# Optimization experiments

Measured on AMD Instinct MI355X. Metric: run time of the kernel, lower is better.

Reference implementation:

```python
import jax, jax.numpy as jnp
import numpy as np
from jax import lax

B = 8192
DEPTH = 4096
SCALES = 3
FLT = 4  # db2 filter length

_DB2_DEC_LO = np.array([-0.12940952255092145, 0.22414386804185735, 0.836516303737469, 0.48296291314469025], dtype=np.float32)
_DB2_DEC_HI = np.array([-0.48296291314469025, 0.836516303737469, 0.22414386804185735, 0.12940952255092145], dtype=np.float32)


def _coeff_lens(depth, flen, scales):
    # mirrors pywt.dwt_coeff_len(n, flen, 'zero') = floor((n + flen - 1) / 2)
    lens = [depth]
    for _ in range(scales):
        lens.append((lens[-1] + flen - 1) // 2)
    lens = lens[1:]
    lens.append(lens[-1])
    return lens  # e.g. [2049, 1026, 514, 514]

WAVE_DEPTH = int(np.sum(_coeff_lens(DEPTH, FLT, SCALES)))  # 4103


def setup_inputs() -> dict:
    key = jax.random.key(0)
    ks = jax.random.split(key, 5)
    x = jax.random.normal(ks[0], (B, DEPTH), dtype=jnp.float32)
    diag_b = 1.0 + 0.1 * jax.random.normal(ks[1], (DEPTH,), dtype=jnp.float32)
    diag_g = 1.0 + 0.1 * jax.random.normal(ks[2], (WAVE_DEPTH,), dtype=jnp.float32)
    diag_s = 1.0 + 0.1 * jax.random.normal(ks[3], (DEPTH,), dtype=jnp.float32)
    dec_lo = jnp.asarray(_DB2_DEC_LO)
    dec_hi = jnp.asarray(_DB2_DEC_HI)
    rec_lo = dec_lo[::-1]
    rec_hi = dec_hi[::-1]
    perm_idx = jax.random.permutation(ks[4], WAVE_DEPTH).astype(jnp.int32)
    return {"x": x, "diag_b": diag_b, "diag_g": diag_g, "diag_s": diag_s,
            "dec_lo": dec_lo, "dec_hi": dec_hi, "rec_lo": rec_lo, "rec_hi": rec_hi,
            "perm_idx": perm_idx}


def _forward(x, diag_b, diag_g, diag_s, dec_lo, dec_hi, rec_lo, rec_hi, perm_idx):
    L = dec_lo.shape[0]
    lens = _coeff_lens(x.shape[-1], L, SCALES)
    # mul_b: diag(vec) matmul == elementwise column scale
    a = x * diag_b
    # multi-level analysis DWT with 'zero' padding: full convolution, keep odd indices
    w_dec = jnp.stack([dec_lo[::-1], dec_hi[::-1]])[:, None, :]  # [2,1,L] (flip: lax does corr)
    details = []
    for _ in range(SCALES):
        y = lax.conv_general_dilated(a[:, None, :], w_dec, (2,), [(L - 2, L - 1)],
                                     dimension_numbers=("NCH", "OIH", "NCH"))
        a, d = y[:, 0, :], y[:, 1, :]
        details.append(d)
    c = jnp.concatenate([a] + details[::-1], axis=-1)  # [B, WAVE_DEPTH], [cA_s, cD_s, ..., cD_1]
    # mul_p: permutation matmul == column gather
    c = c[:, perm_idx]
    # mul_g
    c = c * diag_g
    # coefficient slicing exactly as in the original forward (incl. its start-update rule)
    rev = lens[::-1]
    coeffs = []
    start = 0
    for s_i in range(SCALES + 1):
        stop = start + rev[s_i]
        coeffs.append(c[:, start:stop])
        start = lens[s_i]
    # multi-level reconstruction (idwt, zero mode): zero-upsample, full conv, trim L-2 per side
    a = coeffs[0]
    w_rec = jnp.stack([rec_lo[::-1], rec_hi[::-1]])[None, :, :]  # [1,2,L]
    for d in coeffs[1:]:
        if a.shape[-1] == d.shape[-1] + 1:  # pywt waverec odd-length trim
            a = a[:, :-1]
        xin = jnp.stack([a, d], axis=1)  # [B,2,la]
        a = lax.conv_general_dilated(xin, w_rec, (1,), [(1, 1)], lhs_dilation=(2,),
                                     dimension_numbers=("NCH", "OIH", "NCH"))[:, 0, :]
    # mul_s
    return a * diag_s


def reference(x, diag_b, diag_g, diag_s, dec_lo, dec_hi, rec_lo, rec_hi, perm_idx):
    return _forward(x, diag_b, diag_g, diag_s, dec_lo, dec_hi, rec_lo, rec_hi, perm_idx)
```

## Files before the change

kernel.cpp:

```cpp
#include <hip/hip_runtime.h>


#define NT 512

__global__ __launch_bounds__(NT, 8) void wavelet_fused(
    const float* __restrict__ x,
    const float* __restrict__ diag_b,
    const float* __restrict__ diag_g,
    const float* __restrict__ diag_s,
    const float* __restrict__ dec_lo,
    const float* __restrict__ dec_hi,
    const float* __restrict__ rec_lo,
    const float* __restrict__ rec_hi,
    const int*   __restrict__ perm_idx,
    float* __restrict__ out)
{
    __shared__ __align__(16) float rawA[3088];
    __shared__ __align__(16) float rawC[4112];
    float* const A1 = rawA + 4;
    float* const A2 = rawA + 2060;
    float* const P  = rawA;
    float* const Cc = rawC;
    float* const R1 = rawC;

    const int tid = threadIdx.x;
    const long row = blockIdx.x;

    int4   pq0 = ((const int4*)perm_idx)[tid];
    float4 gq0 = ((const float4*)diag_g)[tid];
    int4   pq1; float4 gq1;
    if (tid < 128) {
        pq1 = ((const int4*)perm_idx)[512 + tid];
        gq1 = ((const float4*)diag_g)[512 + tid];
    }
    int pt = 0; float gt = 0.0f;
    if (tid < 3) { pt = perm_idx[2560 + tid]; gt = diag_g[2560 + tid]; }
    float4 sv0 = ((const float4*)diag_s)[2*tid];
    float4 sv1 = ((const float4*)diag_s)[2*tid + 1];

    const float lo0=dec_lo[0], lo1=dec_lo[1], lo2=dec_lo[2], lo3=dec_lo[3];
    const float hi0=dec_hi[0], hi1=dec_hi[1], hi2=dec_hi[2], hi3=dec_hi[3];
    const float rl0=rec_lo[0], rl1=rec_lo[1], rl2=rec_lo[2], rl3=rec_lo[3];
    const float rh0=rec_hi[0], rh1=rec_hi[1], rh2=rec_hi[2], rh3=rec_hi[3];

    if (tid < 2) rawA[2 + tid]    = 0.0f;
    if (tid < 3) rawA[2053 + tid] = 0.0f;
    if (tid < 2) rawA[2058 + tid] = 0.0f;
    if (tid < 2) rawA[3086 + tid] = 0.0f;

    {
        const float* xr = x + row * 4096;
        float4 xv0 = *(const float4*)(xr + 8*tid);
        float4 xv1 = *(const float4*)(xr + 8*tid + 4);
        float4 bv0 = *(const float4*)(diag_b + 8*tid);
        float4 bv1 = *(const float4*)(diag_b + 8*tid + 4);
        float vm2 = 0.0f, vm1 = 0.0f;
        if (tid > 0) {
            float2 xm = *(const float2*)(xr + 8*tid - 2);
            float2 bm = *(const float2*)(diag_b + 8*tid - 2);
            vm2 = xm.x * bm.x; vm1 = xm.y * bm.y;
        }
        float v0 = xv0.x*bv0.x, v1 = xv0.y*bv0.y, v2 = xv0.z*bv0.z, v3 = xv0.w*bv0.w;
        float v4 = xv1.x*bv1.x, v5 = xv1.y*bv1.y, v6 = xv1.z*bv1.z, v7 = xv1.w*bv1.w;
        float4 av, dv;
        av.x = lo0*v1 + lo1*v0 + lo2*vm1 + lo3*vm2;
        dv.x = hi0*v1 + hi1*v0 + hi2*vm1 + hi3*vm2;
        av.y = lo0*v3 + lo1*v2 + lo2*v1 + lo3*v0;
        dv.y = hi0*v3 + hi1*v2 + hi2*v1 + hi3*v0;
        av.z = lo0*v5 + lo1*v4 + lo2*v3 + lo3*v2;
        dv.z = hi0*v5 + hi1*v4 + hi2*v3 + hi3*v2;
        av.w = lo0*v7 + lo1*v6 + lo2*v5 + lo3*v4;
        dv.w = hi0*v7 + hi1*v6 + hi2*v5 + hi3*v4;
        *(float4*)(A1 + 4*tid) = av;
        *(float4*)(Cc + 2056 + 4*tid) = dv;
        if (tid == 0) {
            float xa = xr[4094]*diag_b[4094], xb = xr[4095]*diag_b[4095];
            A1[2048]        = lo2*xb + lo3*xa;
            Cc[2056 + 2048] = hi2*xb + hi3*xa;
        }
    }
    __syncthreads();

    for (int p = tid; p < 513; p += NT) {
        float2 u0 = *(const float2*)(A1 + 4*p - 2);
        float4 u1 = *(const float4*)(A1 + 4*p);
        float2 ap, dp;
        ap.x = lo0*u1.y + lo1*u1.x + lo2*u0.y + lo3*u0.x;
        dp.x = hi0*u1.y + hi1*u1.x + hi2*u0.y + hi3*u0.x;
        ap.y = lo0*u1.w + lo1*u1.z + lo2*u1.y + lo3*u1.x;
        dp.y = hi0*u1.w + hi1*u1.z + hi2*u1.y + hi3*u1.x;
        *(float2*)(A2 + 2*p)        = ap;
        *(float2*)(Cc + 1028 + 2*p) = dp;
    }
    __syncthreads();

    for (int p = tid; p < 257; p += NT) {
        float2 u0 = *(const float2*)(A2 + 4*p - 2);
        float4 u1 = *(const float4*)(A2 + 4*p);
        float2 ap, dp;
        ap.x = lo0*u1.y + lo1*u1.x + lo2*u0.y + lo3*u0.x;
        dp.x = hi0*u1.y + hi1*u1.x + hi2*u0.y + hi3*u0.x;
        ap.y = lo0*u1.w + lo1*u1.z + lo2*u1.y + lo3*u1.x;
        dp.y = hi0*u1.w + hi1*u1.z + hi2*u1.y + hi3*u1.x;
        *(float2*)(Cc + 2*p)       = ap;
        *(float2*)(Cc + 514 + 2*p) = dp;
    }
    __syncthreads();

    {
        float4 cv;
        cv.x = Cc[pq0.x + (pq0.x >= 2054 ? 2 : 0)] * gq0.x;
        cv.y = Cc[pq0.y + (pq0.y >= 2054 ? 2 : 0)] * gq0.y;
        cv.z = Cc[pq0.z + (pq0.z >= 2054 ? 2 : 0)] * gq0.z;
        cv.w = Cc[pq0.w + (pq0.w >= 2054 ? 2 : 0)] * gq0.w;
        *(float4*)(P + 4*tid) = cv;
        if (tid < 128) {
            float4 cw;
            cw.x = Cc[pq1.x + (pq1.x >= 2054 ? 2 : 0)] * gq1.x;
            cw.y = Cc[pq1.y + (pq1.y >= 2054 ? 2 : 0)] * gq1.y;
            cw.z = Cc[pq1.z + (pq1.z >= 2054 ? 2 : 0)] * gq1.z;
            cw.w = Cc[pq1.w + (pq1.w >= 2054 ? 2 : 0)] * gq1.w;
            *(float4*)(P + 2048 + 4*tid) = cw;
        }
        if (tid < 3)  P[2560 + tid] = Cc[pt + (pt >= 2054 ? 2 : 0)] * gt;
        if (tid == 3) P[2563] = 0.0f;
    }
    __syncthreads();

    if (tid < 257) {
        int p0 = 2 * tid;
        float a0v = P[p0],        a1v = P[p0 + 1],    a2v = P[p0 + 2];
        float d0v = P[2049 + p0], d1v = P[2050 + p0], d2v = P[2051 + p0];
        float4 w;
        w.x = rl2*a0v + rl0*a1v + rh2*d0v + rh0*d1v;
        w.y = rl3*a0v + rl1*a1v + rh3*d0v + rh1*d1v;
        w.z = rl2*a1v + rl0*a2v + rh2*d1v + rh0*d2v;
        w.w = rl3*a1v + rl1*a2v + rh3*d1v + rh1*d2v;
        if (tid < 256) *(float4*)(R1 + 4*tid) = w;
        else           { R1[1024] = w.x; R1[1025] = w.y; }
    }
    __syncthreads();

    {
        const int u = tid;
        float2 q01 = *(const float2*)(R1 + 2*u);
        float2 q23 = *(const float2*)(R1 + 2*u + 2);
        float2 ea  = *(const float2*)(P + 1026 + 2*u);
        float2 eb  = *(const float2*)(P + 1028 + 2*u);
        float e0 = ea.x, e1 = ea.y, e2 = eb.x, e3 = eb.y;
        float s0  = rl2*q01.x + rl0*q01.y + rh2*e0 + rh0*e1;
        float s1v = rl3*q01.x + rl1*q01.y + rh3*e0 + rh1*e1;
        float s2v = rl2*q01.y + rl0*q23.x + rh2*e1 + rh0*e2;
        float s3v = rl3*q01.y + rl1*q23.x + rh3*e1 + rh1*e2;
        float s4  = rl2*q23.x + rl0*q23.y + rh2*e2 + rh0*e3;
        float2 fa = *(const float2*)(P + 514 + 4*u);
        float2 fb = *(const float2*)(P + 516 + 4*u);
        float  f4 = P[518 + 4*u];
        float f0 = fa.x, f1 = fa.y, f2 = fb.x, f3 = fb.y;
        float4 o0, o1;
        o0.x = (rl2*s0  + rl0*s1v + rh2*f0 + rh0*f1) * sv0.x;
        o0.y = (rl3*s0  + rl1*s1v + rh3*f0 + rh1*f1) * sv0.y;
        o0.z = (rl2*s1v + rl0*s2v + rh2*f1 + rh0*f2) * sv0.z;
        o0.w = (rl3*s1v + rl1*s2v + rh3*f1 + rh1*f2) * sv0.w;
        o1.x = (rl2*s2v + rl0*s3v + rh2*f2 + rh0*f3) * sv1.x;
        o1.y = (rl3*s2v + rl1*s3v + rh3*f2 + rh1*f3) * sv1.y;
        o1.z = (rl2*s3v + rl0*s4  + rh2*f3 + rh0*f4) * sv1.z;
        o1.w = (rl3*s3v + rl1*s4  + rh3*f3 + rh1*f4) * sv1.w;
        float4* outr = (float4*)(out + row * 4096);
        outr[2*u]     = o0;
        outr[2*u + 1] = o1;
    }
}

extern "C" void kernel_launch(void* const* d_in, const int* in_sizes, int n_in,
                              void* d_out, int out_size, void* d_ws, size_t ws_size,
                              hipStream_t stream) {
    const float* x       = (const float*)d_in[0];
    const float* diag_b  = (const float*)d_in[1];
    const float* diag_g  = (const float*)d_in[2];
    const float* diag_s  = (const float*)d_in[3];
    const float* dec_lo  = (const float*)d_in[4];
    const float* dec_hi  = (const float*)d_in[5];
    const float* rec_lo  = (const float*)d_in[6];
    const float* rec_hi  = (const float*)d_in[7];
    const int*   perm    = (const int*)d_in[8];
    float* out = (float*)d_out;

    const int B = in_sizes[0] / 4096;
    wavelet_fused<<<B, NT, 0, stream>>>(
        x, diag_b, diag_g, diag_s, dec_lo, dec_hi, rec_lo, rec_hi, perm, out);
}
```

Measured before the change: 261.3 us.

## Compose DWT levels 2-3 into one 10-tap pass and fuse reconstruction levels

Levels two and three of the analysis are merged into a single pass using precomputed composite 10-tap low/high filters applied to the level-1 approximation. Level-2 details are still computed per thread. On the synthesis side, the first reconstruction level is computed in registers inside the second, which removes its shared-memory round trip. This drops two barriers and the A2 buffer, shrinking shared memory, at the cost of redundant FMAs and a few extra boundary special cases.

```diff
diff --git a/kernel.cpp b/kernel.cpp
--- a/kernel.cpp
+++ b/kernel.cpp
@@ -15,13 +15,11 @@
     const int*   __restrict__ perm_idx,
     float* __restrict__ out)
 {
-    __shared__ __align__(16) float rawA[3088];
+    __shared__ __align__(16) float rawA[2568];
     __shared__ __align__(16) float rawC[4112];
-    float* const A1 = rawA + 4;
-    float* const A2 = rawA + 2060;
+    float* const A1 = rawA + 8;
     float* const P  = rawA;
     float* const Cc = rawC;
-    float* const R1 = rawC;
 
     const int tid = threadIdx.x;
     const long row = blockIdx.x;
@@ -43,10 +41,8 @@
     const float rl0=rec_lo[0], rl1=rec_lo[1], rl2=rec_lo[2], rl3=rec_lo[3];
     const float rh0=rec_hi[0], rh1=rec_hi[1], rh2=rec_hi[2], rh3=rec_hi[3];
 
-    if (tid < 2) rawA[2 + tid]    = 0.0f;
-    if (tid < 3) rawA[2053 + tid] = 0.0f;
-    if (tid < 2) rawA[2058 + tid] = 0.0f;
-    if (tid < 2) rawA[3086 + tid] = 0.0f;
+    if (tid < 6) rawA[2 + tid] = 0.0f;
+    if (tid < 7) A1[2049 + tid] = 0.0f;
 
     {
         const float* xr = x + row * 4096;
@@ -79,31 +75,50 @@
             Cc[2056 + 2048] = hi2*xb + hi3*xa;
         }
     }
+
+    float loA[4] = {lo0, lo1, lo2, lo3};
+    float hiA[4] = {hi0, hi1, hi2, hi3};
+    float G[10], H[10];
+    #pragma unroll
+    for (int k = 0; k < 10; ++k) { G[k] = 0.0f; H[k] = 0.0f; }
+    #pragma unroll
+    for (int s = 0; s < 4; ++s)
+        #pragma unroll
+        for (int t = 0; t < 4; ++t) {
+            G[2*s + t] += loA[s] * loA[t];
+            H[2*s + t] += hiA[s] * loA[t];
+        }
     __syncthreads();
 
-    for (int p = tid; p < 513; p += NT) {
-        float2 u0 = *(const float2*)(A1 + 4*p - 2);
-        float4 u1 = *(const float4*)(A1 + 4*p);
-        float2 ap, dp;
-        ap.x = lo0*u1.y + lo1*u1.x + lo2*u0.y + lo3*u0.x;
-        dp.x = hi0*u1.y + hi1*u1.x + hi2*u0.y + hi3*u0.x;
-        ap.y = lo0*u1.w + lo1*u1.z + lo2*u1.y + lo3*u1.x;
-        dp.y = hi0*u1.w + hi1*u1.z + hi2*u1.y + hi3*u1.x;
-        *(float2*)(A2 + 2*p)        = ap;
-        *(float2*)(Cc + 1028 + 2*p) = dp;
-    }
-    __syncthreads();
-
-    for (int p = tid; p < 257; p += NT) {
-        float2 u0 = *(const float2*)(A2 + 4*p - 2);
-        float4 u1 = *(const float4*)(A2 + 4*p);
-        float2 ap, dp;
-        ap.x = lo0*u1.y + lo1*u1.x + lo2*u0.y + lo3*u0.x;
-        dp.x = hi0*u1.y + hi1*u1.x + hi2*u0.y + hi3*u0.x;
-        ap.y = lo0*u1.w + lo1*u1.z + lo2*u1.y + lo3*u1.x;
-        dp.y = hi0*u1.w + hi1*u1.z + hi2*u1.y + hi3*u1.x;
-        *(float2*)(Cc + 2*p)       = ap;
-        *(float2*)(Cc + 514 + 2*p) = dp;
+    {
+        const int p = tid;
+        float W[10];
+        float2 w0 = *(const float2*)(A1 + 4*p - 6);
+        float4 w1 = *(const float4*)(A1 + 4*p - 4);
+        float4 w2 = *(const float4*)(A1 + 4*p);
+        W[0]=w0.x; W[1]=w0.y; W[2]=w1.x; W[3]=w1.y; W[4]=w1.z; W[5]=w1.w;
+        W[6]=w2.x; W[7]=w2.y; W[8]=w2.z; W[9]=w2.w;
+        float a3v = 0.0f, d3v = 0.0f;
+        #pragma unroll
+        for (int j = 0; j < 10; ++j) { a3v += G[9-j]*W[j]; d3v += H[9-j]*W[j]; }
+        Cc[p]       = a3v;
+        Cc[514 + p] = d3v;
+        float2 dd;
+        dd.x = hi0*W[7] + hi1*W[6] + hi2*W[5] + hi3*W[4];
+        dd.y = hi0*W[9] + hi1*W[8] + hi2*W[7] + hi3*W[6];
+        *(float2*)(Cc + 1028 + 2*p) = dd;
+        if (p < 2) {
+            int n = 512 + p;
+            float acc = 0.0f, dcc = 0.0f;
+            #pragma unroll
+            for (int k = 0; k < 10; ++k) {
+                float av = A1[4*n + 3 - k];
+                acc += G[k]*av; dcc += H[k]*av;
+            }
+            Cc[n] = acc; Cc[514 + n] = dcc;
+            int m = 1024 + p;
+            Cc[1028 + m] = hi0*A1[2*m+1] + hi1*A1[2*m] + hi2*A1[2*m-1] + hi3*A1[2*m-2];
+        }
     }
     __syncthreads();
 
@@ -122,37 +137,25 @@
             cw.w = Cc[pq1.w + (pq1.w >= 2054 ? 2 : 0)] * gq1.w;
             *(float4*)(P + 2048 + 4*tid) = cw;
         }
-        if (tid < 3)  P[2560 + tid] = Cc[pt + (pt >= 2054 ? 2 : 0)] * gt;
-        if (tid == 3) P[2563] = 0.0f;
-    }
-    __syncthreads();
-
-    if (tid < 257) {
-        int p0 = 2 * tid;
-        float a0v = P[p0],        a1v = P[p0 + 1],    a2v = P[p0 + 2];
-        float d0v = P[2049 + p0], d1v = P[2050 + p0], d2v = P[2051 + p0];
-        float4 w;
-        w.x = rl2*a0v + rl0*a1v + rh2*d0v + rh0*d1v;
-        w.y = rl3*a0v + rl1*a1v + rh3*d0v + rh1*d1v;
-        w.z = rl2*a1v + rl0*a2v + rh2*d1v + rh0*d2v;
-        w.w = rl3*a1v + rl1*a2v + rh3*d1v + rh1*d2v;
-        if (tid < 256) *(float4*)(R1 + 4*tid) = w;
-        else           { R1[1024] = w.x; R1[1025] = w.y; }
+        if (tid < 3) P[2560 + tid] = Cc[pt + (pt >= 2054 ? 2 : 0)] * gt;
     }
     __syncthreads();
 
     {
         const int u = tid;
-        float2 q01 = *(const float2*)(R1 + 2*u);
-        float2 q23 = *(const float2*)(R1 + 2*u + 2);
-        float2 ea  = *(const float2*)(P + 1026 + 2*u);
-        float2 eb  = *(const float2*)(P + 1028 + 2*u);
-        float e0 = ea.x, e1 = ea.y, e2 = eb.x, e3 = eb.y;
-        float s0  = rl2*q01.x + rl0*q01.y + rh2*e0 + rh0*e1;
-        float s1v = rl3*q01.x + rl1*q01.y + rh3*e0 + rh1*e1;
-        float s2v = rl2*q01.y + rl0*q23.x + rh2*e1 + rh0*e2;
-        float s3v = rl3*q01.y + rl1*q23.x + rh3*e1 + rh1*e2;
-        float s4  = rl2*q23.x + rl0*q23.y + rh2*e2 + rh0*e3;
+        float a0 = P[u], a1v = P[u + 1], a2v = P[u + 2];
+        float b0 = P[2049 + u], b1 = P[2050 + u], b2 = P[2051 + u];
+        float r10 = rl2*a0  + rl0*a1v + rh2*b0 + rh0*b1;
+        float r11 = rl3*a0  + rl1*a1v + rh3*b0 + rh1*b1;
+        float r12 = rl2*a1v + rl0*a2v + rh2*b1 + rh0*b2;
+        float r13 = rl3*a1v + rl1*a2v + rh3*b1 + rh1*b2;
+        float2 ea = *(const float2*)(P + 1026 + 2*u);
+        float2 eb = *(const float2*)(P + 1028 + 2*u);
+        float s0  = rl2*r10 + rl0*r11 + rh2*ea.x + rh0*ea.y;
+        float s1v = rl3*r10 + rl1*r11 + rh3*ea.x + rh1*ea.y;
+        float s2v = rl2*r11 + rl0*r12 + rh2*ea.y + rh0*eb.x;
+        float s3v = rl3*r11 + rl1*r12 + rh3*ea.y + rh1*eb.x;
+        float s4  = rl2*r12 + rl0*r13 + rh2*eb.x + rh0*eb.y;
         float2 fa = *(const float2*)(P + 514 + 4*u);
         float2 fb = *(const float2*)(P + 516 + 4*u);
         float  f4 = P[518 + 4*u];
```

After: 275.3 us. +5.3%, slower.
